# Performance work log

Hardware: AMD Instinct MI355X
Metric: run time of the kernel (lower is better)

The kernel has to match this reference:

```python
import jax, jax.numpy as jnp
import numpy as np

B, C, H, W = 4, 512, 64, 64
CQ = C // 8


def setup_inputs() -> dict:
    key = jax.random.key(0)
    ks = jax.random.split(key, 8)
    s_in = 1.0 / np.sqrt(C)
    return {
        "x": jax.random.normal(ks[0], (B, C, H, W), jnp.float32),
        "wq": jax.random.normal(ks[1], (CQ, C), jnp.float32) * s_in,
        "bq": jax.random.normal(ks[2], (CQ,), jnp.float32) * 0.01,
        "wk": jax.random.normal(ks[3], (CQ, C), jnp.float32) * s_in,
        "bk": jax.random.normal(ks[4], (CQ,), jnp.float32) * 0.01,
        "wv": jax.random.normal(ks[5], (C, C), jnp.float32) * s_in,
        "bv": jax.random.normal(ks[6], (C,), jnp.float32) * 0.01,
        "gamma": jax.random.normal(ks[7], (1,), jnp.float32) * 0.1,
    }


def reference(x, wq, bq, wk, bk, wv, bv, gamma):
    b, c, h, w = x.shape
    n = h * w
    xf = x.reshape(b, c, n)  # [B, C, N]; 1x1 conv == channel matmul
    q = jnp.einsum("oc,bcn->bon", wq, xf) + bq[None, :, None]  # [B, CQ, N]
    k = jnp.einsum("oc,bcn->bon", wk, xf) + bk[None, :, None]  # [B, CQ, N]
    v = jnp.einsum("oc,bcn->bon", wv, xf) + bv[None, :, None]  # [B, C, N]
    energy = jnp.einsum("bcn,bcm->bnm", q, k)  # [B, N, N]
    attn = jax.nn.softmax(energy, axis=-1)
    out = jnp.einsum("bcm,bnm->bcn", v, attn)  # [B, C, N]
    out = out.reshape(b, c, h, w)
    return gamma[0] * out + x
```

## Files before the change

kernel.cpp:

```cpp
#include <hip/hip_runtime.h>
#include <hip/hip_bf16.h>

#define BATCH 4
#define CH    512
#define NPIX  4096
#define LOG2E 1.4426950408889634f

#define BOFF  327680
#define WTOT  328320
#define PSTR  268

typedef float v4f __attribute__((ext_vector_type(4)));
typedef short v8s __attribute__((ext_vector_type(8)));
typedef unsigned short u16;

__device__ __forceinline__ float b2f(u16 v){
    union { unsigned u; float f; } x; x.u = ((unsigned)v) << 16; return x.f;
}
__device__ __forceinline__ u16 f2b(float f){
    union { float f; unsigned u; } x; x.f = f;
    unsigned r = x.u + 0x7fffu + ((x.u >> 16) & 1u);
    return (u16)(r >> 16);
}
__device__ __forceinline__ void f2b2(float a, float b, u16* o){
    union { __hip_bfloat162 v; u16 s[2]; } u;
    u.v = __float22bfloat162_rn(make_float2(a, b));
    o[0] = u.s[0]; o[1] = u.s[1];
}
__device__ __forceinline__ float fexp2(float x){
#if __has_builtin(__builtin_amdgcn_exp2f)
    return __builtin_amdgcn_exp2f(x);
#else
    return exp2f(x);
#endif
}
__device__ __forceinline__ v4f mfma16(v8s a, v8s b, v4f c){
    return __builtin_amdgcn_mfma_f32_16x16x32_bf16(a, b, c, 0, 0, 0);
}
__device__ __forceinline__ float load_s(const void* p, size_t idx, int isf32){
    return isf32 ? ((const float*)p)[idx] : b2f(((const u16*)p)[idx]);
}

__global__ void detect_kernel(const unsigned* __restrict__ x, int* __restrict__ flag){
    __shared__ int cnt;
    if (threadIdx.x == 0) cnt = 0;
    __syncthreads();
    int c = 0;
    for (int i = threadIdx.x; i < 1024; i += 64){
        unsigned e = (x[i] >> 23) & 0xFFu;
        if (e >= 64u && e < 192u) c++;
    }
    atomicAdd(&cnt, c);
    __syncthreads();
    if (threadIdx.x == 0) flag[0] = (cnt > 512) ? 1 : 0;
}

__global__ __launch_bounds__(256) void prep_kernel(
    const void* __restrict__ wq, const void* __restrict__ bq,
    const void* __restrict__ wk, const void* __restrict__ bk,
    const void* __restrict__ wv, const void* __restrict__ bv,
    u16* __restrict__ wall, const int* __restrict__ flag)
{
    const int isf32 = flag[0];
    int i = blockIdx.x * 256 + threadIdx.x;
    if (i >= WTOT) return;
    float v;
    if (i < BOFF){
        int o = i >> 9, c = i & 511;
        if (o < 64)       v = load_s(wq, (size_t)o * 512 + c, isf32);
        else if (o < 128) v = load_s(wk, (size_t)(o - 64) * 512 + c, isf32);
        else              v = load_s(wv, (size_t)(o - 128) * 512 + c, isf32);
    } else {
        int o = i - BOFF;
        if (o < 64)       v = load_s(bq, o, isf32);
        else if (o < 128) v = load_s(bk, o - 64, isf32);
        else              v = load_s(bv, o - 128, isf32);
    }
    wall[i] = f2b(v);
}

__global__ __launch_bounds__(256, 2) void proj_kernel(
    const void* __restrict__ x, const u16* __restrict__ wall,
    u16* __restrict__ Qf, u16* __restrict__ Kf, u16* __restrict__ Vf,
    u16* __restrict__ xbf, const int* __restrict__ flag)
{
    const int isf32 = flag[0];
    const int ntile = blockIdx.x, os = blockIdx.y, b = blockIdx.z;
    const int n0 = ntile * 64;
    const int t = threadIdx.x, lane = t & 63, w = t >> 6, q = lane >> 4, col = lane & 15;

    __shared__ __align__(16) u16 xT[2][64 * 40];

    const int rrow  = t >> 3;
    const int ncol8 = (t & 7) * 8;
    const size_t xbase = (size_t)b * CH * NPIX + n0 + ncol8;

    v4f acc[5][4];
    #pragma unroll
    for (int i = 0; i < 5; i++)
        #pragma unroll
        for (int j = 0; j < 4; j++) acc[i][j] = (v4f){0.f, 0.f, 0.f, 0.f};

    float4 gn0, gn1;

    #define LOADX(cb_) do {                                                  \
        const size_t src = xbase + (size_t)((cb_) * 32 + rrow) * NPIX;       \
        if (isf32){ gn0 = *(const float4*)((const float*)x + src);           \
                    gn1 = *(const float4*)((const float*)x + src + 4); }     \
        else { union { uint4 v; float4 f; } lu;                              \
               lu.v = *(const uint4*)((const u16*)x + src); gn0 = lu.f; }    \
    } while (0)

    #define CVT8(vals_) do {                                                 \
        if (isf32){ f2b2(gn0.x, gn0.y, &vals_[0]); f2b2(gn0.z, gn0.w, &vals_[2]); \
                    f2b2(gn1.x, gn1.y, &vals_[4]); f2b2(gn1.z, gn1.w, &vals_[6]); } \
        else { union { float4 f; uint4 v; } uu; uu.f = gn0;                  \
               *(uint4*)vals_ = uu.v; }                                      \
    } while (0)

    {
        LOADX(0);
        u16 vals[8]; CVT8(vals);
        #pragma unroll
        for (int i = 0; i < 8; i++) xT[0][(ncol8 + i) * 40 + rrow] = vals[i];
        if (os == 0)
            *(uint4*)&xbf[(size_t)(b * CH + rrow) * NPIX + n0 + ncol8] = *(uint4*)vals;
        LOADX(1);
    }
    __syncthreads();

    for (int cb = 0; cb < 16; cb++){
        const int buf = cb & 1;
        const int c0 = cb * 32 + q * 8;

        v8s wf[5];
        #pragma unroll
        for (int ct = 0; ct < 5; ct++)
            wf[ct] = *(const v8s*)&wall[(size_t)(320 * os + 80 * w + 16 * ct + col) * 512 + c0];

        v8s a[4];
        #pragma unroll
        for (int g = 0; g < 4; g++)
            a[g] = *(const v8s*)&xT[buf][(16 * g + col) * 40 + q * 8];

        if (cb < 15){
            u16 vals[8]; CVT8(vals);
            #pragma unroll
            for (int i = 0; i < 8; i++) xT[buf ^ 1][(ncol8 + i) * 40 + rrow] = vals[i];
            if (os == 0)
                *(uint4*)&xbf[(size_t)(b * CH + (cb + 1) * 32 + rrow) * NPIX + n0 + ncol8] = *(uint4*)vals;
            if (cb < 14) LOADX(cb + 2);
        }

        #pragma unroll
        for (int ct = 0; ct < 5; ct++)
            #pragma unroll
            for (int g = 0; g < 4; g++)
                acc[ct][g] = mfma16(a[g], wf[ct], acc[ct][g]);
        __syncthreads();
    }
    #undef LOADX
    #undef CVT8

    const u16* ball = wall + BOFF;
    #pragma unroll
    for (int ct = 0; ct < 5; ct++){
        const int o = 320 * os + 80 * w + 16 * ct + col;
        const float bv_ = b2f(ball[o]);
        #pragma unroll
        for (int g = 0; g < 4; g++){
            const int nb = n0 + 16 * g + 4 * q;
            if (o < 64){
                const int k = o;
                size_t base = (size_t)b * NPIX * 64
                    + ((size_t)((nb >> 4) * 2 + (k >> 5))) * 512
                    + ((k & 31) >> 3) * 128 + (nb & 15) * 8 + (k & 7);
                #pragma unroll
                for (int r = 0; r < 4; r++)
                    Qf[base + r * 8] = f2b((acc[ct][g][r] + bv_) * LOG2E);
            } else if (o < 128){
                const int k = o - 64;
                size_t base = (size_t)b * NPIX * 64
                    + ((size_t)((nb >> 4) * 2 + (k >> 5))) * 512
                    + ((k & 31) >> 3) * 128 + (nb & 15) * 8 + (k & 7);
                #pragma unroll
                for (int r = 0; r < 4; r++)
                    Kf[base + r * 8] = f2b(acc[ct][g][r] + bv_);
            } else {
                const int c = o - 128;
                size_t base = (size_t)b * CH * NPIX
                    + ((size_t)((c >> 4) * 128 + (nb >> 5))) * 512
                    + ((nb & 31) >> 3) * 128 + (c & 15) * 8 + (nb & 7);
                union { uint2 u; u16 s[4]; } ov;
                #pragma unroll
                for (int r = 0; r < 4; r++)
                    ov.s[r] = f2b(acc[ct][g][r] + bv_);
                *(uint2*)&Vf[base] = ov.u;
            }
        }
    }
}

__global__ __launch_bounds__(512, 4) void attn_kernel(
    const u16* __restrict__ Qf, const u16* __restrict__ Kf, const u16* __restrict__ Vf,
    const u16* __restrict__ xbf, const void* __restrict__ gamma,
    void* __restrict__ out, const int* __restrict__ flag)
{
    const int isf32 = flag[0];
    const int bid = blockIdx.x;
    const int csplit = bid & 1;
    const int b      = (bid >> 1) & 3;
    const int ntile  = bid >> 3;
    const int n0 = ntile * 64;

    const int t = threadIdx.x, lane = t & 63, w = t >> 6, q = lane >> 4, col = lane & 15;

    __shared__ __align__(16) u16  Plds[2][64 * PSTR];
    __shared__ __align__(16) float lsum[8][64];

    const u16* Qb = Qf + (size_t)b * NPIX * 64;
    const u16* Kb = Kf + (size_t)b * NPIX * 64;
    const u16* Vb = Vf + (size_t)b * CH * NPIX;

    v8s qa[4][2];
    #pragma unroll
    for (int g = 0; g < 4; g++)
        #pragma unroll
        for (int c2 = 0; c2 < 2; c2++)
            qa[g][c2] = *(const v8s*)&Qb[(size_t)(((n0 >> 4) + g) * 2 + c2) * 512 + lane * 8];

    float lreg[4] = {0.f, 0.f, 0.f, 0.f};

    v4f oacc[2][4];
    #pragma unroll
    for (int i = 0; i < 2; i++)
        #pragma unroll
        for (int j = 0; j < 4; j++) oacc[i][j] = (v4f){0.f, 0.f, 0.f, 0.f};

    const int ms    = 32 * w;
    const int cslab = csplit * 256 + 32 * w;

    for (int it = 0; it < 16; it++){
        const int m0 = it * 256;
        const int buf = it & 1;

        v8s kf[2][2];
        #pragma unroll
        for (int mt = 0; mt < 2; mt++)
            #pragma unroll
            for (int c2 = 0; c2 < 2; c2++)
                kf[mt][c2] = *(const v8s*)&Kb[(size_t)((((m0 + ms) >> 4) + mt) * 2 + c2) * 512 + lane * 8];

        #pragma unroll
        for (int g = 0; g < 4; g++){
            #pragma unroll
            for (int mt = 0; mt < 2; mt++){
                v4f sv = (v4f){-64.f, -64.f, -64.f, -64.f};
                sv = mfma16(kf[mt][0], qa[g][0], sv);
                sv = mfma16(kf[mt][1], qa[g][1], sv);
                float p0 = fexp2(sv[0]), p1 = fexp2(sv[1]);
                float p2 = fexp2(sv[2]), p3 = fexp2(sv[3]);
                lreg[g] += (p0 + p1) + (p2 + p3);
                union { uint2 u; u16 s[4]; } pk;
                f2b2(p0, p1, &pk.s[0]);
                f2b2(p2, p3, &pk.s[2]);
                *(uint2*)&Plds[buf][(16 * g + col) * PSTR + ms + 16 * mt + 4 * q] = pk.u;
            }
        }

        __syncthreads();

        v8s va_c[2];
        #pragma unroll
        for (int ct = 0; ct < 2; ct++)
            va_c[ct] = *(const v8s*)&Vb[(size_t)(((cslab + 16 * ct) >> 4) * 128 + (m0 >> 5)) * 512 + lane * 8];
        #pragma unroll
        for (int kk = 0; kk < 8; kk++){
            v8s va_n[2];
            if (kk < 7){
                #pragma unroll
                for (int ct = 0; ct < 2; ct++)
                    va_n[ct] = *(const v8s*)&Vb[(size_t)(((cslab + 16 * ct) >> 4) * 128 + (m0 >> 5) + kk + 1) * 512 + lane * 8];
            }
            v8s pb[4];
            #pragma unroll
            for (int nt = 0; nt < 4; nt++)
                pb[nt] = *(const v8s*)&Plds[buf][(16 * nt + col) * PSTR + 32 * kk + q * 8];
            #pragma unroll
            for (int ct = 0; ct < 2; ct++)
                #pragma unroll
                for (int nt = 0; nt < 4; nt++)
                    oacc[ct][nt] = mfma16(va_c[ct], pb[nt], oacc[ct][nt]);
            #pragma unroll
            for (int ct = 0; ct < 2; ct++) va_c[ct] = va_n[ct];
        }
    }

    #pragma unroll
    for (int g = 0; g < 4; g++){
        lreg[g] += __shfl_xor(lreg[g], 16);
        lreg[g] += __shfl_xor(lreg[g], 32);
    }
    if (lane < 16){
        #pragma unroll
        for (int g = 0; g < 4; g++)
            lsum[w][16 * g + lane] = lreg[g];
    }
    __syncthreads();

    const float gam = load_s(gamma, 0, isf32);
    float linv[4];
    #pragma unroll
    for (int nt = 0; nt < 4; nt++){
        int nn = 16 * nt + col;
        float l = ((lsum[0][nn] + lsum[1][nn]) + (lsum[2][nn] + lsum[3][nn]))
                + ((lsum[4][nn] + lsum[5][nn]) + (lsum[6][nn] + lsum[7][nn]));
        linv[nt] = gam / l;
    }

    const size_t boff = (size_t)b * CH * NPIX;
    #pragma unroll
    for (int ct = 0; ct < 2; ct++){
        #pragma unroll
        for (int rr = 0; rr < 4; rr++){
            int c = cslab + 16 * ct + 4 * q + rr;
            size_t base = boff + (size_t)c * NPIX + n0;
            #pragma unroll
            for (int nt = 0; nt < 4; nt++){
                int n = 16 * nt + col;
                float o = oacc[ct][nt][rr] * linv[nt] + b2f(xbf[base + n]);
                if (isf32) ((float*)out)[base + n] = o;
                else       ((u16*)out)[base + n]  = f2b(o);
            }
        }
    }
}

extern "C" void kernel_launch(void* const* d_in, const int* in_sizes, int n_in,
                              void* d_out, int out_size, void* d_ws, size_t ws_size,
                              hipStream_t stream)
{
    const void* x     = d_in[0];
    const void* wq    = d_in[1];
    const void* bq    = d_in[2];
    const void* wk    = d_in[3];
    const void* bk    = d_in[4];
    const void* wv    = d_in[5];
    const void* bv    = d_in[6];
    const void* gamma = d_in[7];

    u16* Qf   = (u16*)d_ws;
    u16* Kf   = Qf + (size_t)1048576;
    u16* Vf   = Kf + (size_t)1048576;
    u16* xbf  = Vf + (size_t)8388608;
    u16* wall = xbf + (size_t)8388608;
    int* flag = (int*)(wall + WTOT + 16);

    detect_kernel<<<1, 64, 0, stream>>>((const unsigned*)x, flag);
    prep_kernel<<<(WTOT + 255) / 256, 256, 0, stream>>>(wq, bq, wk, bk, wv, bv, wall, flag);
    proj_kernel<<<dim3(64, 2, BATCH), 256, 0, stream>>>(x, wall, Qf, Kf, Vf, xbf, flag);
    attn_kernel<<<512, 512, 0, stream>>>(Qf, Kf, Vf, xbf, gamma, d_out, flag);
}
```

Baseline: 217.8 us.

## Fold detect/prep kernels into proj and prefetch K fragments in attention loop

Drops the separate dtype-detect and weight-prep kernels. Each proj and attn block now sniffs the input dtype itself, and proj reads and converts the weights and biases from the original tensors inline. The attention loop loads the next iteration's K fragments early, issues the V loads before the score computation, and raises wave priority around the MFMA block. This removes two launches and one weight round-trip through memory. In exchange, every block repeats the detection and the fp32 weight conversion, and the prefetch adds register pressure.

```diff
diff --git a/kernel.cpp b/kernel.cpp
--- a/kernel.cpp
+++ b/kernel.cpp
@@ -5,9 +5,6 @@
 #define CH    512
 #define NPIX  4096
 #define LOG2E 1.4426950408889634f
-
-#define BOFF  327680
-#define WTOT  328320
 #define PSTR  268
 
 typedef float v4f __attribute__((ext_vector_type(4)));
@@ -41,55 +38,38 @@
     return isf32 ? ((const float*)p)[idx] : b2f(((const u16*)p)[idx]);
 }
 
-__global__ void detect_kernel(const unsigned* __restrict__ x, int* __restrict__ flag){
-    __shared__ int cnt;
-    if (threadIdx.x == 0) cnt = 0;
+__device__ __forceinline__ int sniff_isf32(const unsigned* __restrict__ xw,
+                                           int t, int nthr, int* cnt){
+    if (t == 0) *cnt = 0;
     __syncthreads();
     int c = 0;
-    for (int i = threadIdx.x; i < 1024; i += 64){
-        unsigned e = (x[i] >> 23) & 0xFFu;
+    for (int i = t; i < 1024; i += nthr){
+        unsigned e = (xw[i] >> 23) & 0xFFu;
         if (e >= 64u && e < 192u) c++;
     }
-    atomicAdd(&cnt, c);
+    c += __shfl_xor(c, 1);  c += __shfl_xor(c, 2);  c += __shfl_xor(c, 4);
+    c += __shfl_xor(c, 8);  c += __shfl_xor(c, 16); c += __shfl_xor(c, 32);
+    if ((t & 63) == 0) atomicAdd(cnt, c);
     __syncthreads();
-    if (threadIdx.x == 0) flag[0] = (cnt > 512) ? 1 : 0;
-}
-
-__global__ __launch_bounds__(256) void prep_kernel(
-    const void* __restrict__ wq, const void* __restrict__ bq,
-    const void* __restrict__ wk, const void* __restrict__ bk,
-    const void* __restrict__ wv, const void* __restrict__ bv,
-    u16* __restrict__ wall, const int* __restrict__ flag)
+    return (*cnt > 512) ? 1 : 0;
+}
+
+__global__ __launch_bounds__(256, 2) void proj_kernel(
+    const void* __restrict__ x,
+    const void* __restrict__ wqg, const void* __restrict__ bqg,
+    const void* __restrict__ wkg, const void* __restrict__ bkg,
+    const void* __restrict__ wvg, const void* __restrict__ bvg,
+    u16* __restrict__ Qf, u16* __restrict__ Kf, u16* __restrict__ Vf,
+    u16* __restrict__ xbf)
 {
-    const int isf32 = flag[0];
-    int i = blockIdx.x * 256 + threadIdx.x;
-    if (i >= WTOT) return;
-    float v;
-    if (i < BOFF){
-        int o = i >> 9, c = i & 511;
-        if (o < 64)       v = load_s(wq, (size_t)o * 512 + c, isf32);
-        else if (o < 128) v = load_s(wk, (size_t)(o - 64) * 512 + c, isf32);
-        else              v = load_s(wv, (size_t)(o - 128) * 512 + c, isf32);
-    } else {
-        int o = i - BOFF;
-        if (o < 64)       v = load_s(bq, o, isf32);
-        else if (o < 128) v = load_s(bk, o - 64, isf32);
-        else              v = load_s(bv, o - 128, isf32);
-    }
-    wall[i] = f2b(v);
-}
-
-__global__ __launch_bounds__(256, 2) void proj_kernel(
-    const void* __restrict__ x, const u16* __restrict__ wall,
-    u16* __restrict__ Qf, u16* __restrict__ Kf, u16* __restrict__ Vf,
-    u16* __restrict__ xbf, const int* __restrict__ flag)
-{
-    const int isf32 = flag[0];
+    __shared__ __align__(16) u16 xT[2][64 * 40];
+    __shared__ int scnt;
+
+    const int isf32 = sniff_isf32((const unsigned*)x, threadIdx.x, 256, &scnt);
+
     const int ntile = blockIdx.x, os = blockIdx.y, b = blockIdx.z;
     const int n0 = ntile * 64;
     const int t = threadIdx.x, lane = t & 63, w = t >> 6, q = lane >> 4, col = lane & 15;
-
-    __shared__ __align__(16) u16 xT[2][64 * 40];
 
     const int rrow  = t >> 3;
     const int ncol8 = (t & 7) * 8;
@@ -135,8 +115,24 @@
 
         v8s wf[5];
         #pragma unroll
-        for (int ct = 0; ct < 5; ct++)
-            wf[ct] = *(const v8s*)&wall[(size_t)(320 * os + 80 * w + 16 * ct + col) * 512 + c0];
+        for (int ct = 0; ct < 5; ct++){
+            const int o = 320 * os + 80 * w + 16 * ct + col;
+            const void* base; int oo;
+            if (o < 64)       { base = wqg; oo = o; }
+            else if (o < 128) { base = wkg; oo = o - 64; }
+            else              { base = wvg; oo = o - 128; }
+            if (isf32){
+                const float* f = (const float*)base + (size_t)oo * 512 + c0;
+                float4 f0 = *(const float4*)f;
+                float4 f1 = *(const float4*)(f + 4);
+                union { v8s v; u16 s[8]; } uu;
+                f2b2(f0.x, f0.y, &uu.s[0]); f2b2(f0.z, f0.w, &uu.s[2]);
+                f2b2(f1.x, f1.y, &uu.s[4]); f2b2(f1.z, f1.w, &uu.s[6]);
+                wf[ct] = uu.v;
+            } else {
+                wf[ct] = *(const v8s*)((const u16*)base + (size_t)oo * 512 + c0);
+            }
+        }
 
         v8s a[4];
         #pragma unroll
@@ -162,11 +158,13 @@
     #undef LOADX
     #undef CVT8
 
-    const u16* ball = wall + BOFF;
     #pragma unroll
     for (int ct = 0; ct < 5; ct++){
         const int o = 320 * os + 80 * w + 16 * ct + col;
-        const float bv_ = b2f(ball[o]);
+        float bias;
+        if (o < 64)       bias = load_s(bqg, o, isf32);
+        else if (o < 128) bias = load_s(bkg, o - 64, isf32);
+        else              bias = load_s(bvg, o - 128, isf32);
         #pragma unroll
         for (int g = 0; g < 4; g++){
             const int nb = n0 + 16 * g + 4 * q;
@@ -177,7 +175,7 @@
                     + ((k & 31) >> 3) * 128 + (nb & 15) * 8 + (k & 7);
                 #pragma unroll
                 for (int r = 0; r < 4; r++)
-                    Qf[base + r * 8] = f2b((acc[ct][g][r] + bv_) * LOG2E);
+                    Qf[base + r * 8] = f2b((acc[ct][g][r] + bias) * LOG2E);
             } else if (o < 128){
                 const int k = o - 64;
                 size_t base = (size_t)b * NPIX * 64
@@ -185,7 +183,7 @@
                     + ((k & 31) >> 3) * 128 + (nb & 15) * 8 + (k & 7);
                 #pragma unroll
                 for (int r = 0; r < 4; r++)
-                    Kf[base + r * 8] = f2b(acc[ct][g][r] + bv_);
+                    Kf[base + r * 8] = f2b(acc[ct][g][r] + bias);
             } else {
                 const int c = o - 128;
                 size_t base = (size_t)b * CH * NPIX
@@ -194,7 +192,7 @@
                 union { uint2 u; u16 s[4]; } ov;
                 #pragma unroll
                 for (int r = 0; r < 4; r++)
-                    ov.s[r] = f2b(acc[ct][g][r] + bv_);
+                    ov.s[r] = f2b(acc[ct][g][r] + bias);
                 *(uint2*)&Vf[base] = ov.u;
             }
         }
@@ -202,11 +200,17 @@
 }
 
 __global__ __launch_bounds__(512, 4) void attn_kernel(
+    const void* __restrict__ x,
     const u16* __restrict__ Qf, const u16* __restrict__ Kf, const u16* __restrict__ Vf,
     const u16* __restrict__ xbf, const void* __restrict__ gamma,
-    void* __restrict__ out, const int* __restrict__ flag)
+    void* __restrict__ out)
 {
-    const int isf32 = flag[0];
+    __shared__ __align__(16) u16  Plds[2][64 * PSTR];
+    __shared__ __align__(16) float lsum[8][64];
+    __shared__ int scnt;
+
+    const int isf32 = sniff_isf32((const unsigned*)x, threadIdx.x, 512, &scnt);
+
     const int bid = blockIdx.x;
     const int csplit = bid & 1;
     const int b      = (bid >> 1) & 3;
@@ -215,9 +219,6 @@
 
     const int t = threadIdx.x, lane = t & 63, w = t >> 6, q = lane >> 4, col = lane & 15;
 
-    __shared__ __align__(16) u16  Plds[2][64 * PSTR];
-    __shared__ __align__(16) float lsum[8][64];
-
     const u16* Qb = Qf + (size_t)b * NPIX * 64;
     const u16* Kb = Kf + (size_t)b * NPIX * 64;
     const u16* Vb = Vf + (size_t)b * CH * NPIX;
@@ -240,16 +241,21 @@
     const int ms    = 32 * w;
     const int cslab = csplit * 256 + 32 * w;
 
+    v8s kf[2][2];
+    #pragma unroll
+    for (int mt = 0; mt < 2; mt++)
+        #pragma unroll
+        for (int c2 = 0; c2 < 2; c2++)
+            kf[mt][c2] = *(const v8s*)&Kb[(size_t)(((ms >> 4) + mt) * 2 + c2) * 512 + lane * 8];
+
     for (int it = 0; it < 16; it++){
         const int m0 = it * 256;
         const int buf = it & 1;
 
-        v8s kf[2][2];
-        #pragma unroll
-        for (int mt = 0; mt < 2; mt++)
-            #pragma unroll
-            for (int c2 = 0; c2 < 2; c2++)
-                kf[mt][c2] = *(const v8s*)&Kb[(size_t)((((m0 + ms) >> 4) + mt) * 2 + c2) * 512 + lane * 8];
+        v8s va_c[2];
+        #pragma unroll
+        for (int ct = 0; ct < 2; ct++)
+            va_c[ct] = *(const v8s*)&Vb[(size_t)(((cslab + 16 * ct) >> 4) * 128 + (m0 >> 5)) * 512 + lane * 8];
 
         #pragma unroll
         for (int g = 0; g < 4; g++){
@@ -268,12 +274,18 @@
             }
         }
 
+        v8s kfn[2][2];
+        if (it < 15){
+            const int m1 = m0 + 256;
+            #pragma unroll
+            for (int mt = 0; mt < 2; mt++)
+                #pragma unroll
+                for (int c2 = 0; c2 < 2; c2++)
+                    kfn[mt][c2] = *(const v8s*)&Kb[(size_t)((((m1 + ms) >> 4) + mt) * 2 + c2) * 512 + lane * 8];
+        }
+
         __syncthreads();
 
-        v8s va_c[2];
-        #pragma unroll
-        for (int ct = 0; ct < 2; ct++)
-            va_c[ct] = *(const v8s*)&Vb[(size_t)(((cslab + 16 * ct) >> 4) * 128 + (m0 >> 5)) * 512 + lane * 8];
         #pragma unroll
         for (int kk = 0; kk < 8; kk++){
             v8s va_n[2];
@@ -286,13 +298,23 @@
             #pragma unroll
             for (int nt = 0; nt < 4; nt++)
                 pb[nt] = *(const v8s*)&Plds[buf][(16 * nt + col) * PSTR + 32 * kk + q * 8];
+            __builtin_amdgcn_s_setprio(1);
             #pragma unroll
             for (int ct = 0; ct < 2; ct++)
                 #pragma unroll
                 for (int nt = 0; nt < 4; nt++)
                     oacc[ct][nt] = mfma16(va_c[ct], pb[nt], oacc[ct][nt]);
+            __builtin_amdgcn_s_setprio(0);
             #pragma unroll
             for (int ct = 0; ct < 2; ct++) va_c[ct] = va_n[ct];
+        }
+
+        if (it < 15){
+            #pragma unroll
+            for (int mt = 0; mt < 2; mt++)
+                #pragma unroll
+                for (int c2 = 0; c2 < 2; c2++)
+                    kf[mt][c2] = kfn[mt][c2];
         }
     }
 
@@ -353,11 +375,8 @@
     u16* Kf   = Qf + (size_t)1048576;
     u16* Vf   = Kf + (size_t)1048576;
     u16* xbf  = Vf + (size_t)8388608;
-    u16* wall = xbf + (size_t)8388608;
-    int* flag = (int*)(wall + WTOT + 16);
-
-    detect_kernel<<<1, 64, 0, stream>>>((const unsigned*)x, flag);
-    prep_kernel<<<(WTOT + 255) / 256, 256, 0, stream>>>(wq, bq, wk, bk, wv, bv, wall, flag);
-    proj_kernel<<<dim3(64, 2, BATCH), 256, 0, stream>>>(x, wall, Qf, Kf, Vf, xbf, flag);
-    attn_kernel<<<512, 512, 0, stream>>>(Qf, Kf, Vf, xbf, gamma, d_out, flag);
-}
+
+    proj_kernel<<<dim3(64, 2, BATCH), 256, 0, stream>>>(
+        x, wq, bq, wk, bk, wv, bv, Qf, Kf, Vf, xbf);
+    attn_kernel<<<512, 512, 0, stream>>>(x, Qf, Kf, Vf, xbf, gamma, d_out);
+}
```

Result: slower. 233.4 us (+7.2%).
